# Optimization experiments

Measured on AMD Instinct MI355X. Metric: run time of the kernel, lower is better.

Reference implementation:

```python
import jax, jax.numpy as jnp
import numpy as np

L, D, H, G = 3, 64, 4, 64            # layers, hidden_dim, heads, num_graphs
N, E = 20000, 320000                  # nodes, edges
HD = H * D                            # heads * out_channels = 256
DENSE = 256
EPS = 1e-5


def setup_inputs() -> dict:
    key = jax.random.key(0)
    ks = jax.random.split(key, 32)
    s = 0.05
    f32 = jnp.float32
    inp = {
        "x": jax.random.normal(ks[0], (N, D), f32),
        "edge_attr": jax.random.normal(ks[1], (E, D), f32),
        "edge_index": jax.random.randint(ks[2], (2, E), 0, N, dtype=jnp.int32),
        "batch": ((jnp.arange(N, dtype=jnp.int32) * G) // N).astype(jnp.int32),
        # per-layer TransformerConv params (stacked over layer dim)
        "Wq": jax.random.normal(ks[3], (L, D, HD), f32) * s,
        "bq": jnp.zeros((L, HD), f32),
        "Wk": jax.random.normal(ks[4], (L, D, HD), f32) * s,
        "bk": jnp.zeros((L, HD), f32),
        "Wv": jax.random.normal(ks[5], (L, D, HD), f32) * s,
        "bv": jnp.zeros((L, HD), f32),
        "We": jax.random.normal(ks[6], (L, D, HD), f32) * s,   # lin_edge (no bias in PyG)
        "Wskip": jax.random.normal(ks[7], (L, D, HD), f32) * s,
        "bskip": jnp.zeros((L, HD), f32),
        "bn_gamma": jnp.ones((L, HD), f32),
        "bn_beta": jnp.zeros((L, HD), f32),
        "Wt": jax.random.normal(ks[8], (L, HD, D), f32) * s,   # transf_layers
        "bt": jnp.zeros((L, D), f32),
        # MLP head
        "W1": jax.random.normal(ks[9], (2 * D, DENSE), f32) * s,
        "b1": jnp.zeros((DENSE,), f32),
        "W2": jax.random.normal(ks[10], (DENSE, DENSE // 2), f32) * s,
        "b2": jnp.zeros((DENSE // 2,), f32),
        "W3": jax.random.normal(ks[11], (DENSE // 2, 1), f32) * s,
        "b3": jnp.zeros((1,), f32),
    }
    return inp


def _transformer_conv(x, edge_attr, src, dst, Wq, bq, Wk, bk, Wv, bv, We, Wskip, bskip):
    # PyG TransformerConv, concat=True, beta=False, root_weight=True, eval (no attn dropout)
    q = (x @ Wq + bq).reshape(N, H, D)[dst]                 # [E,H,C]
    k = (x @ Wk + bk).reshape(N, H, D)[src]                 # [E,H,C]
    v = (x @ Wv + bv).reshape(N, H, D)[src]                 # [E,H,C]
    e = (edge_attr @ We).reshape(E, H, D)                   # [E,H,C]
    k = k + e
    logits = (q * k).sum(-1) / jnp.sqrt(jnp.asarray(D, x.dtype))  # [E,H]
    m = jax.ops.segment_max(logits, dst, num_segments=N)    # stable softmax per dst node
    p = jnp.exp(logits - m[dst])
    z = jax.ops.segment_sum(p, dst, num_segments=N)
    w = p / z[dst]                                          # [E,H]
    msg = w[..., None] * (v + e)                            # [E,H,C]
    agg = jax.ops.segment_sum(msg, dst, num_segments=N).reshape(N, HD)
    return agg + x @ Wskip + bskip                          # [N, H*C]


def _batchnorm(h, gamma, beta):
    mu = h.mean(0)
    var = h.var(0)  # biased, as torch BN uses for normalization
    return (h - mu) * jax.lax.rsqrt(var + EPS) * gamma + beta


def reference(x, edge_attr, edge_index, batch, Wq, bq, Wk, bk, Wv, bv, We, Wskip,
              bskip, bn_gamma, bn_beta, Wt, bt, W1, b1, W2, b2, W3, b3):
    src, dst = edge_index[0], edge_index[1]
    counts = jax.ops.segment_sum(jnp.ones((N,), x.dtype), batch, num_segments=G)
    rep = jnp.zeros((G, 2 * D), x.dtype)
    for i in range(L):
        h = _transformer_conv(x, edge_attr, src, dst, Wq[i], bq[i], Wk[i], bk[i],
                              Wv[i], bv[i], We[i], Wskip[i], bskip[i])
        h = _batchnorm(h, bn_gamma[i], bn_beta[i])
        x = jax.nn.relu(h @ Wt[i] + bt[i])                  # [N, D]
        gmx = jax.ops.segment_max(x, batch, num_segments=G)
        gav = jax.ops.segment_sum(x, batch, num_segments=G) / counts[:, None]
        rep = rep + jnp.concatenate([gmx, gav], axis=1)     # sum of per-layer reps
    out = jax.nn.relu(rep @ W1 + b1)
    out = jax.nn.relu(out @ W2 + b2)
    return out @ W3 + b3                                    # [G, 1]
```

## Files before the change

### kernel.cpp

```cpp
#include <hip/hip_runtime.h>
#include <math.h>
#include <float.h>

#define N_NODES 20000
#define N_PAD 20032
#define N_EDGES 320000
#define NGRAPH 64
#define NLAYER 3
#define BN_EPS 1e-5f

typedef short bf16x8 __attribute__((ext_vector_type(8)));
typedef float f32x4 __attribute__((ext_vector_type(4)));

__device__ inline unsigned short f2bf(float f) {
    unsigned int u = __float_as_uint(f);
    unsigned int r = u + 0x7FFF + ((u >> 16) & 1);
    return (unsigned short)(r >> 16);
}
__device__ inline float bf2f(unsigned short s) {
    return __uint_as_float((unsigned int)s << 16);
}

__global__ void count_kernel(const int* __restrict__ ei, int* __restrict__ cnt) {
    int e = blockIdx.x * blockDim.x + threadIdx.x;
    if (e < N_EDGES) atomicAdd(&cnt[ei[N_EDGES + e]], 1);
}

__global__ void scan_kernel(const int* __restrict__ cnt, int* __restrict__ rowptr) {
    __shared__ int sh[256];
    int t = threadIdx.x;
    const int CH = (N_NODES + 255) / 256;
    int base = t * CH;
    int s = 0;
    for (int i = 0; i < CH; i++) { int idx = base + i; if (idx < N_NODES) s += cnt[idx]; }
    sh[t] = s;
    __syncthreads();
    for (int off = 1; off < 256; off <<= 1) {
        int v = sh[t];
        int add = (t >= off) ? sh[t - off] : 0;
        __syncthreads();
        sh[t] = v + add;
        __syncthreads();
    }
    int run = sh[t] - s;
    for (int i = 0; i < CH; i++) {
        int idx = base + i;
        if (idx < N_NODES) { rowptr[idx] = run; run += cnt[idx]; }
    }
    if (t == 255) rowptr[N_NODES] = sh[255];
}

__global__ void fill_kernel(const int* __restrict__ ei, const int* __restrict__ rowptr,
                            int* __restrict__ cur, int* __restrict__ eidx,
                            int* __restrict__ esrc) {
    int e = blockIdx.x * blockDim.x + threadIdx.x;
    if (e < N_EDGES) {
        int dst = ei[N_EDGES + e];
        int pos = atomicAdd(&cur[dst], 1);
        int slot = rowptr[dst] + pos;
        eidx[slot] = e;
        esrc[slot] = ei[e];
    }
}

__global__ void permute_ea_b_kernel(const float* __restrict__ edge_attr,
                                    const int* __restrict__ eidx,
                                    unsigned short* __restrict__ eaPb) {
    int idx = blockIdx.x * blockDim.x + threadIdx.x;
    if (idx < N_EDGES * 16) {
        int j = idx >> 4, c4 = idx & 15;
        float4 v = *(const float4*)(edge_attr + (size_t)eidx[j] * 64 + c4 * 4);
        ((ushort4*)eaPb)[idx] = make_ushort4(f2bf(v.x), f2bf(v.y), f2bf(v.z), f2bf(v.w));
    }
}

__global__ void wallt2_kernel(const float* __restrict__ Wq, const float* __restrict__ Wk,
                              const float* __restrict__ Wv, const float* __restrict__ Ws,
                              const float* __restrict__ We,
                              const float* __restrict__ bq, const float* __restrict__ bk,
                              const float* __restrict__ bv, const float* __restrict__ bs,
                              unsigned short* __restrict__ WallT, float* __restrict__ ball) {
    int c = blockIdx.x, l = blockIdx.y, k = threadIdx.x;
    int seg = c >> 8, ci = c & 255;
    if (seg < 4) {
        const float* W; const float* b;
        switch (seg) {
            case 0:  W = Wq; b = bq; break;
            case 1:  W = Wk; b = bk; break;
            case 2:  W = Wv; b = bv; break;
            default: W = Ws; b = bs; break;
        }
        WallT[(size_t)l * 81920 + c * 64 + k] = f2bf(W[l * 16384 + k * 256 + ci]);
        if (k == 0) ball[l * 1280 + c] = b[l * 256 + ci];
    } else {
        int h = ci >> 6, d = ci & 63;
        const float* Wql = Wq + l * 16384;
        const float* Wel = We + l * 16384;
        float acc = 0.f;
        for (int cc = 0; cc < 64; cc++)
            acc += Wql[k * 256 + h * 64 + cc] * Wel[d * 256 + h * 64 + cc];
        WallT[(size_t)l * 81920 + c * 64 + k] = f2bf(acc);
        if (k == 0) {
            const float* bql = bq + l * 256;
            float ab = 0.f;
            for (int cc = 0; cc < 64; cc++) ab += bql[h * 64 + cc] * Wel[d * 256 + h * 64 + cc];
            ball[l * 1280 + c] = ab;
        }
    }
}

__global__ void xtobf_kernel(const float* __restrict__ x, unsigned short* __restrict__ xbf) {
    int i4 = blockIdx.x * 256 + threadIdx.x;
    if (i4 >= N_PAD * 64 / 4) return;
    int n = i4 >> 4;
    ushort4 o;
    if (n < N_NODES) {
        float4 v = ((const float4*)x)[i4];
        o = make_ushort4(f2bf(v.x), f2bf(v.y), f2bf(v.z), f2bf(v.w));
    } else o = make_ushort4(0, 0, 0, 0);
    ((ushort4*)xbf)[i4] = o;
}

__global__ __launch_bounds__(256) void gemm_qkvsu4_kernel(
    const unsigned short* __restrict__ xbf,
    const unsigned short* __restrict__ WallT,
    const float* __restrict__ ball,
    unsigned short* __restrict__ qbf, unsigned char* __restrict__ kvf8,
    unsigned short* __restrict__ sbf, unsigned short* __restrict__ ubf) {
    int t = threadIdx.x, wid = t >> 6, lane = t & 63;
    int lrow = lane & 15, lk = lane >> 4;

    bf16x8 bfrag[2][4][2];
    float bias[2][4];
    int kind[2];
    unsigned short* outb[2]; int obase[2];
#pragma unroll
    for (int cg = 0; cg < 2; cg++) {
        int ys = blockIdx.y * 2 + cg;
        int col0 = ys * 64;
        int q = ys & 3;
        if (ys < 4)       { kind[cg] = 0; outb[cg] = qbf; obase[cg] = q * 64; }
        else if (ys < 8)  { kind[cg] = 1; outb[cg] = nullptr; obase[cg] = q * 64; }
        else if (ys < 12) { kind[cg] = 2; outb[cg] = nullptr; obase[cg] = q * 64; }
        else if (ys < 16) { kind[cg] = 0; outb[cg] = sbf; obase[cg] = q * 64; }
        else              { kind[cg] = 0; outb[cg] = ubf; obase[cg] = q * 64; }
#pragma unroll
        for (int ct = 0; ct < 4; ct++) {
#pragma unroll
            for (int kc = 0; kc < 2; kc++)
                bfrag[cg][ct][kc] = *(const bf16x8*)(WallT +
                    (size_t)(col0 + ct * 16 + lrow) * 64 + kc * 32 + lk * 8);
            bias[cg][ct] = ball[col0 + ct * 16 + lrow];
        }
    }

    for (int nc = blockIdx.x; nc < N_PAD / 64; nc += gridDim.x) {
        int n0 = nc * 64 + wid * 16;
        bf16x8 a0 = *(const bf16x8*)(xbf + (size_t)(n0 + lrow) * 64 + lk * 8);
        bf16x8 a1 = *(const bf16x8*)(xbf + (size_t)(n0 + lrow) * 64 + 32 + lk * 8);
#pragma unroll
        for (int cg = 0; cg < 2; cg++) {
#pragma unroll
            for (int ct = 0; ct < 4; ct++) {
                f32x4 acc = {bias[cg][ct], bias[cg][ct], bias[cg][ct], bias[cg][ct]};
                acc = __builtin_amdgcn_mfma_f32_16x16x32_bf16(a0, bfrag[cg][ct][0], acc, 0, 0, 0);
                acc = __builtin_amdgcn_mfma_f32_16x16x32_bf16(a1, bfrag[cg][ct][1], acc, 0, 0, 0);
                int cl = ct * 16 + lrow;
#pragma unroll
                for (int r = 0; r < 4; r++) {
                    int n = n0 + lk * 4 + r;
                    if (n < N_NODES) {
                        if (kind[cg] == 0) {
                            outb[cg][(size_t)n * 256 + obase[cg] + cl] = f2bf(acc[r]);
                        } else {
                            unsigned int pk = __builtin_amdgcn_cvt_pk_fp8_f32(
                                acc[r], acc[r], 0, false);
                            int ch = obase[cg] + cl;
                            kvf8[(size_t)n * 512 + 2 * ch + (kind[cg] - 1)] =
                                (unsigned char)pk;
                        }
                    }
                }
            }
        }
    }
}

__global__ __launch_bounds__(256) void attn10_kernel(
    const unsigned short* __restrict__ eaPb,
    const float* __restrict__ ea_f32,
    const int* __restrict__ eaidx,
    const int* __restrict__ rowptr, const int* __restrict__ esrc,
    const unsigned short* __restrict__ qbf, const unsigned short* __restrict__ ubf,
    const unsigned char* __restrict__ kvf8,
    const unsigned short* __restrict__ sbf,
    unsigned short* __restrict__ hskb,
    unsigned short* __restrict__ raccb) {
    int t = threadIdx.x;
    int wid = t >> 6, lane = t & 63;
    int c4 = lane * 4;
    int ec4 = (lane & 15) * 4;
    for (int n = blockIdx.x * 4 + wid; n < N_NODES; n += gridDim.x * 4) {
        ushort4 qu = *(const ushort4*)(qbf + (size_t)n * 256 + c4);
        ushort4 uu = *(const ushort4*)(ubf + (size_t)n * 256 + c4);
        float4 q4 = make_float4(bf2f(qu.x), bf2f(qu.y), bf2f(qu.z), bf2f(qu.w));
        float4 u4 = make_float4(bf2f(uu.x), bf2f(uu.y), bf2f(uu.z), bf2f(uu.w));
        int j0 = rowptr[n];
        int cnt = rowptr[n + 1] - j0;
        float l = 0.f;
        float4 a4 = make_float4(0.f, 0.f, 0.f, 0.f), r4 = a4;

        for (int base = 0; base < cnt; base += 64) {
            int nb = cnt - base;
            if (nb > 64) nb = 64;
            int jb = j0 + base;
            int srcv = (lane < nb) ? esrc[jb + lane] : 0;
            uint2 kvA = make_uint2(0, 0), kvB = kvA;
            float4 eA = make_float4(0.f, 0.f, 0.f, 0.f), eB = eA;

#define LOADE(KV, EV, JJ) do { \
        int _s = __builtin_amdgcn_readlane(srcv, (JJ)); \
        KV = *(const uint2*)(kvf8 + (size_t)_s * 512 + c4 * 2); \
        int _j = jb + (JJ); \
        if (eaPb) { ushort4 _e = *(const ushort4*)(eaPb + (size_t)_j * 64 + ec4); \
                    EV = make_float4(bf2f(_e.x), bf2f(_e.y), bf2f(_e.z), bf2f(_e.w)); } \
        else { float4 _f = *(const float4*)(ea_f32 + (size_t)eaidx[_j] * 64 + ec4); \
               EV = _f; } \
    } while (0)

#define PROC(KV, EV) do { \
        float K0 = __builtin_amdgcn_cvt_f32_fp8(KV.x, 0); \
        float V0 = __builtin_amdgcn_cvt_f32_fp8(KV.x, 1); \
        float K1 = __builtin_amdgcn_cvt_f32_fp8(KV.x, 2); \
        float V1 = __builtin_amdgcn_cvt_f32_fp8(KV.x, 3); \
        float K2 = __builtin_amdgcn_cvt_f32_fp8(KV.y, 0); \
        float V2 = __builtin_amdgcn_cvt_f32_fp8(KV.y, 1); \
        float K3 = __builtin_amdgcn_cvt_f32_fp8(KV.y, 2); \
        float V3 = __builtin_amdgcn_cvt_f32_fp8(KV.y, 3); \
        float p = q4.x * K0 + q4.y * K1 + q4.z * K2 + q4.w * K3 \
                + u4.x * EV.x + u4.y * EV.y + u4.z * EV.z + u4.w * EV.w; \
        p += __shfl_xor(p, 1); p += __shfl_xor(p, 2); \
        p += __shfl_xor(p, 4); p += __shfl_xor(p, 8); \
        p = __expf(p * 0.125f); \
        l += p; \
        a4.x += p * V0; a4.y += p * V1; a4.z += p * V2; a4.w += p * V3; \
        r4.x += p * EV.x; r4.y += p * EV.y; r4.z += p * EV.z; r4.w += p * EV.w; \
    } while (0)

            if (nb > 0) LOADE(kvA, eA, 0);
            if (nb > 1) LOADE(kvB, eB, 1);
            int jj = 0;
            for (; jj + 1 < nb; jj += 2) {
                uint2 kv0 = kvA; float4 e0 = eA;
                if (jj + 2 < nb) LOADE(kvA, eA, jj + 2);
                PROC(kv0, e0);
                uint2 kv1 = kvB; float4 e1 = eB;
                if (jj + 3 < nb) LOADE(kvB, eB, jj + 3);
                PROC(kv1, e1);
            }
            if (jj < nb) PROC(kvA, eA);
#undef LOADE
#undef PROC
        }
        float inv = (l > 0.f) ? 1.f / l : 0.f;
        ushort4 su = *(const ushort4*)(sbf + (size_t)n * 256 + c4);
        *(ushort4*)(hskb + (size_t)n * 256 + c4) = make_ushort4(
            f2bf(a4.x * inv + bf2f(su.x)), f2bf(a4.y * inv + bf2f(su.y)),
            f2bf(a4.z * inv + bf2f(su.z)), f2bf(a4.w * inv + bf2f(su.w)));
        *(ushort4*)(raccb + (size_t)n * 256 + c4) = make_ushort4(
            f2bf(r4.x * inv), f2bf(r4.y * inv), f2bf(r4.z * inv), f2bf(r4.w * inv));
    }
}

__global__ __launch_bounds__(256) void msgbn2_kernel(
    const unsigned short* __restrict__ raccb, const float* __restrict__ We,
    const unsigned short* __restrict__ hskb, unsigned short* __restrict__ hbf,
    float* __restrict__ statsL) {
    int t = threadIdx.x;
    float wcol[64];
#pragma unroll
    for (int d = 0; d < 64; d++) wcol[d] = We[d * 256 + t];
    int hoff = t & 192;
    float s = 0.f, s2 = 0.f;
    for (int n = blockIdx.x * 4; n < N_NODES; n += gridDim.x * 4) {
#pragma unroll
        for (int ni = 0; ni < 4; ni++) {
            const unsigned short* rrow = raccb + (size_t)(n + ni) * 256 + hoff;
            float acc = 0.f;
#pragma unroll
            for (int d4 = 0; d4 < 64; d4 += 4) {
                ushort4 r4 = *(const ushort4*)(rrow + d4);
                acc += bf2f(r4.x) * wcol[d4] + bf2f(r4.y) * wcol[d4 + 1]
                     + bf2f(r4.z) * wcol[d4 + 2] + bf2f(r4.w) * wcol[d4 + 3];
            }
            float hv = bf2f(hskb[(size_t)(n + ni) * 256 + t]) + acc;
            hbf[(size_t)(n + ni) * 256 + t] = f2bf(hv);
            s += hv; s2 += hv * hv;
        }
    }
    int base = (blockIdx.x & 7) * 512;
    atomicAdd(&statsL[base + t], s);
    atomicAdd(&statsL[base + 256 + t], s2);
}

__global__ __launch_bounds__(256) void xform5_kernel(
    const unsigned short* __restrict__ hbf,
    const float* __restrict__ Wt,
    const float* __restrict__ gamma, const float* __restrict__ beta,
    const float* __restrict__ bt,
    const float* __restrict__ statsL,
    unsigned short* __restrict__ xbf,
    float* __restrict__ poolmx, float* __restrict__ poolsm, int layer) {
    __shared__ float xt[64][65];
    __shared__ float red[4][2][2][64];
    __shared__ float aL[256], bbL[256], partb[256], biasL[64];
    int t = threadIdx.x, wid = t >> 6, lane = t & 63;
    int lrow = lane & 15, lk = lane >> 4;

    {
        float sum = 0.f, sq = 0.f;
#pragma unroll
        for (int s = 0; s < 8; s++) {
            sum += statsL[s * 512 + t];
            sq  += statsL[s * 512 + 256 + t];
        }
        float mean = sum * (1.f / N_NODES);
        float var = sq * (1.f / N_NODES) - mean * mean;
        float a = rsqrtf(var + BN_EPS) * gamma[t];
        aL[t] = a;
        bbL[t] = beta[t] - mean * a;
    }
    __syncthreads();
    {
        float p = 0.f;
        int o = t & 63, kq = (t >> 6) * 64;
        for (int kk = kq; kk < kq + 64; kk++) p += bbL[kk] * Wt[kk * 64 + o];
        partb[t] = p;
    }
    __syncthreads();
    if (t < 64) biasL[t] = bt[t] + partb[t] + partb[64 + t] + partb[128 + t] + partb[192 + t];
    __syncthreads();

    bf16x8 bfrag[4][8];
#pragma unroll
    for (int ct = 0; ct < 4; ct++) {
        int o = ct * 16 + lrow;
#pragma unroll
        for (int kc = 0; kc < 8; kc++) {
            short tmp[8];
#pragma unroll
            for (int i = 0; i < 8; i++) {
                int k = kc * 32 + lk * 8 + i;
                tmp[i] = (short)f2bf(aL[k] * Wt[k * 64 + o]);
            }
            bfrag[ct][kc] = *(bf16x8*)tmp;
        }
    }
    float bias[4];
#pragma unroll
    for (int ct = 0; ct < 4; ct++) bias[ct] = biasL[ct * 16 + lrow];

    for (int nc = blockIdx.x; nc < N_PAD / 64; nc += gridDim.x) {
        int n0 = nc * 64;
        int nw = n0 + wid * 16;
        f32x4 acc[4];
#pragma unroll
        for (int ct = 0; ct < 4; ct++)
            acc[ct] = {bias[ct], bias[ct], bias[ct], bias[ct]};
#pragma unroll
        for (int kc = 0; kc < 8; kc++) {
            bf16x8 a = *(const bf16x8*)(hbf + (size_t)(nw + lrow) * 256 + kc * 32 + lk * 8);
#pragma unroll
            for (int ct = 0; ct < 4; ct++)
                acc[ct] = __builtin_amdgcn_mfma_f32_16x16x32_bf16(a, bfrag[ct][kc], acc[ct], 0, 0, 0);
        }
#pragma unroll
        for (int ct = 0; ct < 4; ct++) {
            int c = ct * 16 + lrow;
#pragma unroll
            for (int r = 0; r < 4; r++) {
                int n = nw + lk * 4 + r;
                float v = fmaxf(acc[ct][r], 0.f);
                xt[wid * 16 + lk * 4 + r][c] = v;
                if (n < N_NODES) xbf[(size_t)n * 64 + c] = f2bf(v);
            }
        }
        __syncthreads();
        int g0 = (n0 * 64) / 20000;
        int b = ((20000 * (g0 + 1) + 63) >> 6) - n0;
        if (b > 64) b = 64;
        {
            int ch = t & 63, rp = t >> 6;
            float mx0 = 0.f, sm0 = 0.f, mx1 = 0.f, sm1 = 0.f;
            for (int r = rp * 16; r < rp * 16 + 16; r++) {
                if (n0 + r < N_NODES) {
                    float v = xt[r][ch];
                    if (r < b) { mx0 = fmaxf(mx0, v); sm0 += v; }
                    else       { mx1 = fmaxf(mx1, v); sm1 += v; }
                }
            }
            red[rp][0][0][ch] = mx0; red[rp][0][1][ch] = sm0;
            red[rp][1][0][ch] = mx1; red[rp][1][1][ch] = sm1;
        }
        __syncthreads();
        if (t < 128) {
            int seg = t >> 6, ch = t & 63;
            float m = red[0][seg][0][ch], s = red[0][seg][1][ch];
#pragma unroll
            for (int w = 1; w < 4; w++) {
                m = fmaxf(m, red[w][seg][0][ch]);
                s += red[w][seg][1][ch];
            }
            int g = g0 + seg;
            bool valid = (seg == 0) || (b < 64 && g < NGRAPH);
            if (valid) {
                atomicMax((unsigned int*)&poolmx[(layer * NGRAPH + g) * 64 + ch],
                          __float_as_uint(m));
                atomicAdd(&poolsm[(layer * NGRAPH + g) * 64 + ch], s);
            }
        }
        __syncthreads();
    }
}

__global__ __launch_bounds__(256) void head_kernel(
    const float* __restrict__ poolmx, const float* __restrict__ poolsm,
    const float* __restrict__ W1, const float* __restrict__ b1,
    const float* __restrict__ W2, const float* __restrict__ b2,
    const float* __restrict__ W3, const float* __restrict__ b3,
    float* __restrict__ out) {
    int g = blockIdx.x, t = threadIdx.x;
    __shared__ float repL[128], o1sh[256], o2sh[128];
    if (t < 128) {
        int d = t & 63;
        int start = (N_NODES * g + 63) >> 6;
        int end = (N_NODES * (g + 1) + 63) >> 6;
        float v = 0.f;
        if (t < 64) {
#pragma unroll
            for (int l = 0; l < NLAYER; l++) v += poolmx[(l * NGRAPH + g) * 64 + d];
        } else {
            float inv = 1.f / (float)(end - start);
#pragma unroll
            for (int l = 0; l < NLAYER; l++) v += poolsm[(l * NGRAPH + g) * 64 + d] * inv;
        }
        repL[t] = v;
    }
    __syncthreads();
    float a1 = b1[t];
    for (int k = 0; k < 128; k++) a1 += repL[k] * W1[k * 256 + t];
    o1sh[t] = fmaxf(a1, 0.f);
    __syncthreads();
    if (t < 128) {
        float a2 = b2[t];
        for (int k = 0; k < 256; k++) a2 += o1sh[k] * W2[k * 128 + t];
        o2sh[t] = fmaxf(a2, 0.f);
    }
    __syncthreads();
    if (t < 64) {
        float p = o2sh[t] * W3[t] + o2sh[t + 64] * W3[t + 64];
#pragma unroll
        for (int off = 32; off; off >>= 1) p += __shfl_xor(p, off);
        if (t == 0) out[g] = p + b3[0];
    }
}

extern "C" void kernel_launch(void* const* d_in, const int* in_sizes, int n_in,
                              void* d_out, int out_size, void* d_ws, size_t ws_size,
                              hipStream_t stream) {
    const float* x         = (const float*)d_in[0];
    const float* edge_attr = (const float*)d_in[1];
    const int*   ei        = (const int*)d_in[2];
    const float* Wq  = (const float*)d_in[4];
    const float* bq  = (const float*)d_in[5];
    const float* Wk  = (const float*)d_in[6];
    const float* bk  = (const float*)d_in[7];
    const float* Wv  = (const float*)d_in[8];
    const float* bv  = (const float*)d_in[9];
    const float* We  = (const float*)d_in[10];
    const float* Wsk = (const float*)d_in[11];
    const float* bsk = (const float*)d_in[12];
    const float* gam = (const float*)d_in[13];
    const float* bet = (const float*)d_in[14];
    const float* Wt  = (const float*)d_in[15];
    const float* bt  = (const float*)d_in[16];
    const float* W1  = (const float*)d_in[17];
    const float* b1  = (const float*)d_in[18];
    const float* W2  = (const float*)d_in[19];
    const float* b2  = (const float*)d_in[20];
    const float* W3  = (const float*)d_in[21];
    const float* b3  = (const float*)d_in[22];
    float* out = (float*)d_out;

    char* ws = (char*)d_ws;
    size_t off = 0;
    auto alloc = [&](size_t bytes) -> char* {
        char* p = ws + off;
        off += (bytes + 255) & ~(size_t)255;
        return p;
    };
    int*   rowptr = (int*)alloc((N_NODES + 1) * sizeof(int));
    int*   eidx   = (int*)alloc((size_t)N_EDGES * sizeof(int));
    int*   esrc   = (int*)alloc(((size_t)N_EDGES + 64) * sizeof(int));
    unsigned short* qbf  = (unsigned short*)alloc((size_t)N_NODES * 256 * 2);
    unsigned char*  kvf8 = (unsigned char*)alloc((size_t)N_NODES * 512);
    unsigned short* sbf  = (unsigned short*)alloc((size_t)N_NODES * 256 * 2);
    unsigned short* ubf  = (unsigned short*)alloc((size_t)N_NODES * 256 * 2);
    unsigned short* hskb = (unsigned short*)alloc((size_t)N_NODES * 256 * 2);
    unsigned short* raccb= (unsigned short*)alloc((size_t)N_NODES * 256 * 2);
    unsigned short* hbf  = (unsigned short*)alloc((size_t)N_PAD * 256 * 2);
    unsigned short* xbf  = (unsigned short*)alloc((size_t)N_PAD * 64 * 2);
    unsigned short* WallT = (unsigned short*)alloc((size_t)NLAYER * 81920 * 2);
    float* ball   = (float*)alloc((size_t)NLAYER * 1280 * sizeof(float));
    size_t zero_off = off;
    int*   cur1   = (int*)alloc(N_NODES * sizeof(int));
    int*   cur2   = (int*)alloc(N_NODES * sizeof(int));
    float* statsA = (float*)alloc((size_t)NLAYER * 8 * 512 * sizeof(float));
    float* poolmx = (float*)alloc((size_t)NLAYER * NGRAPH * 64 * sizeof(float));
    float* poolsm = (float*)alloc((size_t)NLAYER * NGRAPH * 64 * sizeof(float));
    size_t zero_bytes = off - zero_off;
    unsigned short* eaPb = (unsigned short*)alloc((size_t)N_EDGES * 64 * 2);
    bool perm = (off <= ws_size);

    hipMemsetAsync(ws + zero_off, 0, zero_bytes, stream);

    count_kernel<<<(N_EDGES + 255) / 256, 256, 0, stream>>>(ei, cur1);
    scan_kernel<<<1, 256, 0, stream>>>(cur1, rowptr);
    fill_kernel<<<(N_EDGES + 255) / 256, 256, 0, stream>>>(ei, rowptr, cur2, eidx, esrc);
    if (perm) {
        permute_ea_b_kernel<<<(N_EDGES * 16 + 255) / 256, 256, 0, stream>>>(
            edge_attr, eidx, eaPb);
    }

    wallt2_kernel<<<dim3(1280, NLAYER), 64, 0, stream>>>(
        Wq, Wk, Wv, Wsk, We, bq, bk, bv, bsk, WallT, ball);
    xtobf_kernel<<<(N_PAD * 64 / 4 + 255) / 256, 256, 0, stream>>>(x, xbf);

    for (int i = 0; i < NLAYER; i++) {
        gemm_qkvsu4_kernel<<<dim3(79, 10), 256, 0, stream>>>(
            xbf, WallT + (size_t)i * 81920, ball + i * 1280, qbf, kvf8, sbf, ubf);

        attn10_kernel<<<2500, 256, 0, stream>>>(
            perm ? eaPb : (const unsigned short*)nullptr, edge_attr,
            eidx, rowptr, esrc, qbf, ubf, kvf8, sbf, hskb, raccb);

        msgbn2_kernel<<<1250, 256, 0, stream>>>(
            raccb, We + i * 16384, hskb, hbf, statsA + (size_t)i * 4096);

        xform5_kernel<<<157, 256, 0, stream>>>(
            hbf, Wt + i * 16384, gam + i * 256, bet + i * 256, bt + i * 64,
            statsA + (size_t)i * 4096, xbf, poolmx, poolsm, i);
    }

    head_kernel<<<64, 256, 0, stream>>>(poolmx, poolsm, W1, b1, W2, b2, W3, b3, out);
}
```

Before: 584.1 us.

## Fuse edge-message projection and BN stats into attention kernel; merge prep kernels

The attention kernel now does the per-node raccum×We projection, skip add, bf16 store of h and BatchNorm sum/sumsq accumulation itself, using a transposed bf16 copy of We held in LDS. This removes the separate msgbn kernel and the hskb/raccb intermediate global round-trips. The weight-transpose and x-to-bf16 kernels are also merged into a single prep launch. In exchange, every attention block reloads and transposes We (about 35KB of LDS) and adds two block barriers per 4-node step, which can lower occupancy and add stalls from load imbalance between waves.

```diff
diff --git a/kernel.cpp b/kernel.cpp
--- a/kernel.cpp
+++ b/kernel.cpp
@@ -74,51 +74,56 @@
     }
 }
 
-__global__ void wallt2_kernel(const float* __restrict__ Wq, const float* __restrict__ Wk,
-                              const float* __restrict__ Wv, const float* __restrict__ Ws,
-                              const float* __restrict__ We,
-                              const float* __restrict__ bq, const float* __restrict__ bk,
-                              const float* __restrict__ bv, const float* __restrict__ bs,
-                              unsigned short* __restrict__ WallT, float* __restrict__ ball) {
-    int c = blockIdx.x, l = blockIdx.y, k = threadIdx.x;
-    int seg = c >> 8, ci = c & 255;
-    if (seg < 4) {
-        const float* W; const float* b;
-        switch (seg) {
-            case 0:  W = Wq; b = bq; break;
-            case 1:  W = Wk; b = bk; break;
-            case 2:  W = Wv; b = bv; break;
-            default: W = Ws; b = bs; break;
-        }
-        WallT[(size_t)l * 81920 + c * 64 + k] = f2bf(W[l * 16384 + k * 256 + ci]);
-        if (k == 0) ball[l * 1280 + c] = b[l * 256 + ci];
+__global__ void prep_kernel(const float* __restrict__ Wq, const float* __restrict__ Wk,
+                            const float* __restrict__ Wv, const float* __restrict__ Ws,
+                            const float* __restrict__ We,
+                            const float* __restrict__ bq, const float* __restrict__ bk,
+                            const float* __restrict__ bv, const float* __restrict__ bs,
+                            const float* __restrict__ x,
+                            unsigned short* __restrict__ WallT, float* __restrict__ ball,
+                            unsigned short* __restrict__ xbf) {
+    int bid = blockIdx.x, k = threadIdx.x;
+    if (bid < 1280 * NLAYER) {
+        int l = bid / 1280, c = bid % 1280;
+        int seg = c >> 8, ci = c & 255;
+        if (seg < 4) {
+            const float* W; const float* b;
+            switch (seg) {
+                case 0:  W = Wq; b = bq; break;
+                case 1:  W = Wk; b = bk; break;
+                case 2:  W = Wv; b = bv; break;
+                default: W = Ws; b = bs; break;
+            }
+            WallT[(size_t)l * 81920 + c * 64 + k] = f2bf(W[l * 16384 + k * 256 + ci]);
+            if (k == 0) ball[l * 1280 + c] = b[l * 256 + ci];
+        } else {
+            int h = ci >> 6, d = ci & 63;
+            const float* Wql = Wq + l * 16384;
+            const float* Wel = We + l * 16384;
+            float acc = 0.f;
+            for (int cc = 0; cc < 64; cc++)
+                acc += Wql[k * 256 + h * 64 + cc] * Wel[d * 256 + h * 64 + cc];
+            WallT[(size_t)l * 81920 + c * 64 + k] = f2bf(acc);
+            if (k == 0) {
+                const float* bql = bq + l * 256;
+                float ab = 0.f;
+                for (int cc = 0; cc < 64; cc++)
+                    ab += bql[h * 64 + cc] * Wel[d * 256 + h * 64 + cc];
+                ball[l * 1280 + c] = ab;
+            }
+        }
     } else {
-        int h = ci >> 6, d = ci & 63;
-        const float* Wql = Wq + l * 16384;
-        const float* Wel = We + l * 16384;
-        float acc = 0.f;
-        for (int cc = 0; cc < 64; cc++)
-            acc += Wql[k * 256 + h * 64 + cc] * Wel[d * 256 + h * 64 + cc];
-        WallT[(size_t)l * 81920 + c * 64 + k] = f2bf(acc);
-        if (k == 0) {
-            const float* bql = bq + l * 256;
-            float ab = 0.f;
-            for (int cc = 0; cc < 64; cc++) ab += bql[h * 64 + cc] * Wel[d * 256 + h * 64 + cc];
-            ball[l * 1280 + c] = ab;
-        }
-    }
-}
-
-__global__ void xtobf_kernel(const float* __restrict__ x, unsigned short* __restrict__ xbf) {
-    int i4 = blockIdx.x * 256 + threadIdx.x;
-    if (i4 >= N_PAD * 64 / 4) return;
-    int n = i4 >> 4;
-    ushort4 o;
-    if (n < N_NODES) {
-        float4 v = ((const float4*)x)[i4];
-        o = make_ushort4(f2bf(v.x), f2bf(v.y), f2bf(v.z), f2bf(v.w));
-    } else o = make_ushort4(0, 0, 0, 0);
-    ((ushort4*)xbf)[i4] = o;
+        int i4 = (bid - 1280 * NLAYER) * 64 + k;
+        if (i4 < N_PAD * 16) {
+            int n = i4 >> 4;
+            ushort4 o;
+            if (n < N_NODES) {
+                float4 v = ((const float4*)x)[i4];
+                o = make_ushort4(f2bf(v.x), f2bf(v.y), f2bf(v.z), f2bf(v.w));
+            } else o = make_ushort4(0, 0, 0, 0);
+            ((ushort4*)xbf)[i4] = o;
+        }
+    }
 }
 
 __global__ __launch_bounds__(256) void gemm_qkvsu4_kernel(
@@ -186,7 +191,7 @@
     }
 }
 
-__global__ __launch_bounds__(256) void attn10_kernel(
+__global__ __launch_bounds__(256) void attn12_kernel(
     const unsigned short* __restrict__ eaPb,
     const float* __restrict__ ea_f32,
     const int* __restrict__ eaidx,
@@ -194,13 +199,28 @@
     const unsigned short* __restrict__ qbf, const unsigned short* __restrict__ ubf,
     const unsigned char* __restrict__ kvf8,
     const unsigned short* __restrict__ sbf,
-    unsigned short* __restrict__ hskb,
-    unsigned short* __restrict__ raccb) {
+    const float* __restrict__ We,
+    unsigned short* __restrict__ hbf,
+    float* __restrict__ statsL) {
+    __shared__ unsigned short WeLT[256][68];
+    __shared__ float accL[4][256];
+    __shared__ float raccL[4][256];
     int t = threadIdx.x;
     int wid = t >> 6, lane = t & 63;
     int c4 = lane * 4;
     int ec4 = (lane & 15) * 4;
-    for (int n = blockIdx.x * 4 + wid; n < N_NODES; n += gridDim.x * 4) {
+
+    for (int i = t; i < 16384; i += 256) {
+        int c = i & 255, d = i >> 8;
+        WeLT[c][d] = f2bf(We[d * 256 + c]);
+    }
+    __syncthreads();
+
+    float bns = 0.f, bns2 = 0.f;
+    int h64 = t & 192;
+
+    for (int base = blockIdx.x * 4; base < N_NODES; base += gridDim.x * 4) {
+        int n = base + wid;
         ushort4 qu = *(const ushort4*)(qbf + (size_t)n * 256 + c4);
         ushort4 uu = *(const ushort4*)(ubf + (size_t)n * 256 + c4);
         float4 q4 = make_float4(bf2f(qu.x), bf2f(qu.y), bf2f(qu.z), bf2f(qu.w));
@@ -210,10 +230,10 @@
         float l = 0.f;
         float4 a4 = make_float4(0.f, 0.f, 0.f, 0.f), r4 = a4;
 
-        for (int base = 0; base < cnt; base += 64) {
-            int nb = cnt - base;
+        for (int eb = 0; eb < cnt; eb += 64) {
+            int nb = cnt - eb;
             if (nb > 64) nb = 64;
-            int jb = j0 + base;
+            int jb = j0 + eb;
             int srcv = (lane < nb) ? esrc[jb + lane] : 0;
             uint2 kvA = make_uint2(0, 0), kvB = kvA;
             float4 eA = make_float4(0.f, 0.f, 0.f, 0.f), eB = eA;
@@ -224,8 +244,7 @@
         int _j = jb + (JJ); \
         if (eaPb) { ushort4 _e = *(const ushort4*)(eaPb + (size_t)_j * 64 + ec4); \
                     EV = make_float4(bf2f(_e.x), bf2f(_e.y), bf2f(_e.z), bf2f(_e.w)); } \
-        else { float4 _f = *(const float4*)(ea_f32 + (size_t)eaidx[_j] * 64 + ec4); \
-               EV = _f; } \
+        else { EV = *(const float4*)(ea_f32 + (size_t)eaidx[_j] * 64 + ec4); } \
     } while (0)
 
 #define PROC(KV, EV) do { \
@@ -264,43 +283,33 @@
         }
         float inv = (l > 0.f) ? 1.f / l : 0.f;
         ushort4 su = *(const ushort4*)(sbf + (size_t)n * 256 + c4);
-        *(ushort4*)(hskb + (size_t)n * 256 + c4) = make_ushort4(
-            f2bf(a4.x * inv + bf2f(su.x)), f2bf(a4.y * inv + bf2f(su.y)),
-            f2bf(a4.z * inv + bf2f(su.z)), f2bf(a4.w * inv + bf2f(su.w)));
-        *(ushort4*)(raccb + (size_t)n * 256 + c4) = make_ushort4(
-            f2bf(r4.x * inv), f2bf(r4.y * inv), f2bf(r4.z * inv), f2bf(r4.w * inv));
-    }
-}
-
-__global__ __launch_bounds__(256) void msgbn2_kernel(
-    const unsigned short* __restrict__ raccb, const float* __restrict__ We,
-    const unsigned short* __restrict__ hskb, unsigned short* __restrict__ hbf,
-    float* __restrict__ statsL) {
-    int t = threadIdx.x;
-    float wcol[64];
-#pragma unroll
-    for (int d = 0; d < 64; d++) wcol[d] = We[d * 256 + t];
-    int hoff = t & 192;
-    float s = 0.f, s2 = 0.f;
-    for (int n = blockIdx.x * 4; n < N_NODES; n += gridDim.x * 4) {
+        accL[wid][c4 + 0] = a4.x * inv + bf2f(su.x);
+        accL[wid][c4 + 1] = a4.y * inv + bf2f(su.y);
+        accL[wid][c4 + 2] = a4.z * inv + bf2f(su.z);
+        accL[wid][c4 + 3] = a4.w * inv + bf2f(su.w);
+        *(float4*)(raccL[wid] + c4) = make_float4(r4.x * inv, r4.y * inv,
+                                                  r4.z * inv, r4.w * inv);
+        __syncthreads();
+
 #pragma unroll
         for (int ni = 0; ni < 4; ni++) {
-            const unsigned short* rrow = raccb + (size_t)(n + ni) * 256 + hoff;
-            float acc = 0.f;
-#pragma unroll
-            for (int d4 = 0; d4 < 64; d4 += 4) {
-                ushort4 r4 = *(const ushort4*)(rrow + d4);
-                acc += bf2f(r4.x) * wcol[d4] + bf2f(r4.y) * wcol[d4 + 1]
-                     + bf2f(r4.z) * wcol[d4 + 2] + bf2f(r4.w) * wcol[d4 + 3];
-            }
-            float hv = bf2f(hskb[(size_t)(n + ni) * 256 + t]) + acc;
-            hbf[(size_t)(n + ni) * 256 + t] = f2bf(hv);
-            s += hv; s2 += hv * hv;
-        }
-    }
-    int base = (blockIdx.x & 7) * 512;
-    atomicAdd(&statsL[base + t], s);
-    atomicAdd(&statsL[base + 256 + t], s2);
+            float msg = 0.f;
+#pragma unroll
+            for (int d4 = 0; d4 < 16; d4++) {
+                float4 rv = *(const float4*)(raccL[ni] + h64 + d4 * 4);
+                ushort4 wv = *(const ushort4*)(&WeLT[t][d4 * 4]);
+                msg += rv.x * bf2f(wv.x) + rv.y * bf2f(wv.y)
+                     + rv.z * bf2f(wv.z) + rv.w * bf2f(wv.w);
+            }
+            float hv = accL[ni][t] + msg;
+            hbf[(size_t)(base + ni) * 256 + t] = f2bf(hv);
+            bns += hv; bns2 += hv * hv;
+        }
+        __syncthreads();
+    }
+    int sbase = (blockIdx.x & 7) * 512;
+    atomicAdd(&statsL[sbase + t], bns);
+    atomicAdd(&statsL[sbase + 256 + t], bns2);
 }
 
 __global__ __launch_bounds__(256) void xform5_kernel(
@@ -506,8 +515,6 @@
     unsigned char*  kvf8 = (unsigned char*)alloc((size_t)N_NODES * 512);
     unsigned short* sbf  = (unsigned short*)alloc((size_t)N_NODES * 256 * 2);
     unsigned short* ubf  = (unsigned short*)alloc((size_t)N_NODES * 256 * 2);
-    unsigned short* hskb = (unsigned short*)alloc((size_t)N_NODES * 256 * 2);
-    unsigned short* raccb= (unsigned short*)alloc((size_t)N_NODES * 256 * 2);
     unsigned short* hbf  = (unsigned short*)alloc((size_t)N_PAD * 256 * 2);
     unsigned short* xbf  = (unsigned short*)alloc((size_t)N_PAD * 64 * 2);
     unsigned short* WallT = (unsigned short*)alloc((size_t)NLAYER * 81920 * 2);
@@ -532,20 +539,17 @@
             edge_attr, eidx, eaPb);
     }
 
-    wallt2_kernel<<<dim3(1280, NLAYER), 64, 0, stream>>>(
-        Wq, Wk, Wv, Wsk, We, bq, bk, bv, bsk, WallT, ball);
-    xtobf_kernel<<<(N_PAD * 64 / 4 + 255) / 256, 256, 0, stream>>>(x, xbf);
+    prep_kernel<<<1280 * NLAYER + (N_PAD * 16 + 63) / 64, 64, 0, stream>>>(
+        Wq, Wk, Wv, Wsk, We, bq, bk, bv, bsk, x, WallT, ball, xbf);
 
     for (int i = 0; i < NLAYER; i++) {
         gemm_qkvsu4_kernel<<<dim3(79, 10), 256, 0, stream>>>(
             xbf, WallT + (size_t)i * 81920, ball + i * 1280, qbf, kvf8, sbf, ubf);
 
-        attn10_kernel<<<2500, 256, 0, stream>>>(
+        attn12_kernel<<<2500, 256, 0, stream>>>(
             perm ? eaPb : (const unsigned short*)nullptr, edge_attr,
-            eidx, rowptr, esrc, qbf, ubf, kvf8, sbf, hskb, raccb);
-
-        msgbn2_kernel<<<1250, 256, 0, stream>>>(
-            raccb, We + i * 16384, hskb, hbf, statsA + (size_t)i * 4096);
+            eidx, rowptr, esrc, qbf, ubf, kvf8, sbf,
+            We + i * 16384, hbf, statsA + (size_t)i * 4096);
 
         xform5_kernel<<<157, 256, 0, stream>>>(
             hbf, Wt + i * 16384, gam + i * 256, bet + i * 256, bt + i * 64,
```

Measured after the change: 663.5 us. 1.14x slower.
